# Optimization experiments

Measured on AMD Instinct MI355X. Metric: run time of the kernel, lower is better.

Reference implementation:

```python
import jax, jax.numpy as jnp
import numpy as np

B, C_IN, C_OUT, H, W, K, NK = 16, 256, 256, 64, 64, 3, 2
EPS = 1e-8


def setup_inputs() -> dict:
    key = jax.random.key(0)
    k1, k2, k3, k4 = jax.random.split(key, 4)
    x = jax.random.normal(k1, (B, C_IN, H, W), dtype=jnp.float32)
    mod = jax.random.normal(k2, (B, C_IN), dtype=jnp.float32)
    kernel_mod = jax.random.normal(k3, (B, NK), dtype=jnp.float32)
    # kernel bank: [num_conv_kernels, dim_out, dim_in, k, k] (kaiming-ish scale)
    weights = jax.random.normal(k4, (NK, C_OUT, C_IN, K, K), dtype=jnp.float32) / np.sqrt(C_IN * K * K)
    gamma = jnp.ones((C_OUT,), dtype=jnp.float32)
    return {"x": x, "mod": mod, "kernel_mod": kernel_mod, "weights": weights, "gamma": gamma}


def _block(x, mod, kernel_mod, weights, gamma):
    # adaptive kernel selection: softmax-mix the kernel bank per sample
    attn = jax.nn.softmax(kernel_mod, axis=-1)                       # [b, n]
    w = jnp.einsum('bn,noikl->boikl', attn, weights)                 # [b, o, i, k, k]
    # style modulation over input channels
    w = w * (mod[:, None, :, None, None] + 1.0)
    # demodulation
    denom = jnp.clip(jnp.sum(w * w, axis=(2, 3, 4), keepdims=True), EPS)
    w = w * jax.lax.rsqrt(denom)
    # per-sample conv (groups=b trick in torch) -> vmap over batch
    def conv_one(fmap, wb):
        return jax.lax.conv_general_dilated(
            fmap[None], wb, window_strides=(1, 1), padding='SAME',
            dimension_numbers=('NCHW', 'OIHW', 'NCHW'))[0]
    y = jax.vmap(conv_one)(x, w)                                     # [b, o, h, w]
    # RMSNorm over channel dim: F.normalize(x, dim=1) * gamma * sqrt(dim)
    norm = jnp.sqrt(jnp.sum(y * y, axis=1, keepdims=True))
    y = y / jnp.maximum(norm, 1e-12)
    y = y * gamma[None, :, None, None] * (gamma.shape[0] ** 0.5)
    # SiLU
    return y * jax.nn.sigmoid(y)


def reference(x, mod, kernel_mod, weights, gamma):
    return _block(x, mod, kernel_mod, weights, gamma)
```

## Files before the change

### kernel.cpp

```cpp
#include <hip/hip_runtime.h>
#include <math.h>


typedef __attribute__((ext_vector_type(8))) short short8;
typedef __attribute__((ext_vector_type(16))) float f32x16;

#define GLL16(src, dst)                                                       \
  __builtin_amdgcn_global_load_lds(                                           \
      (const __attribute__((address_space(1))) unsigned int*)(src),           \
      (__attribute__((address_space(3))) unsigned int*)(dst), 16, 0, 0)

static __device__ __forceinline__ unsigned short f2bf(float v) {
  union { float f; unsigned u; } u;
  u.f = v;
  unsigned r = u.u + 0x7FFF + ((u.u >> 16) & 1);
  return (unsigned short)(r >> 16);
}

__global__ __launch_bounds__(256) void wprep(
    const float* __restrict__ mod, const float* __restrict__ kmod,
    const float* __restrict__ weights, unsigned short* __restrict__ wq) {
  int blk = blockIdx.x;
  int b = blk >> 5, oq = blk & 31;
  int t = threadIdx.x;
  int o_l = t >> 5, its = t & 31;
  int o = oq * 8 + o_l;

  float k0 = kmod[b * 2 + 0], k1 = kmod[b * 2 + 1];
  float mx = fmaxf(k0, k1);
  float e0 = expf(k0 - mx), e1 = expf(k1 - mx);
  float ai = 1.0f / (e0 + e1);
  float a0 = e0 * ai, a1 = e1 * ai;

  float wv[9][8];
  float s = 0.0f;
  const float* w0 = &weights[((size_t)o * 256 + its * 8) * 9];
  const float* w1 = w0 + 589824;
#pragma unroll
  for (int e = 0; e < 8; ++e) {
    float f = mod[b * 256 + its * 8 + e] + 1.0f;
#pragma unroll
    for (int j = 0; j < 9; ++j) {
      float v = (a0 * w0[e * 9 + j] + a1 * w1[e * 9 + j]) * f;
      wv[j][e] = v;
      s = fmaf(v, v, s);
    }
  }

  __shared__ float red[8][32];
  __shared__ float scl[8];
  red[o_l][its] = s;
  __syncthreads();
  if (t < 8) {
    float tot = 0.0f;
#pragma unroll
    for (int k = 0; k < 32; ++k) tot += red[t][k];
    scl[t] = rsqrtf(fmaxf(tot, 1e-8f));
  }
  __syncthreads();
  float sc = scl[o_l];

  int c = its >> 1, io = its & 1;
  int oh = o >> 7, mf = (o >> 5) & 3;
  int lane2 = (o & 31) + io * 32;
  size_t cbase = ((size_t)(b * 16 + c)) * 36864 + oh * 2048 + mf * 512 + lane2 * 8;
#pragma unroll
  for (int j = 0; j < 9; ++j) {
    short8 pk;
#pragma unroll
    for (int e = 0; e < 8; ++e) pk[e] = (short)f2bf(wv[j][e] * sc);
    *(short8*)(wq + cbase + j * 4096) = pk;
  }
}

__global__ __launch_bounds__(256) void xprep(
    const float* __restrict__ x, unsigned short* __restrict__ xq) {
  int blk = blockIdx.x;
  int rowp = blk % 66;
  int bc = blk / 66;
  int b = bc >> 4, c = bc & 15;
  int t = threadIdx.x;
  size_t obase = (size_t)blk * 1056;

  if (rowp == 0 || rowp == 65) {
    for (int idx = t; idx < 1056; idx += 256) xq[obase + idx] = 0;
    return;
  }
  __shared__ __align__(16) unsigned short xs2[1056];
  int row = rowp - 1;
  for (int idx = t; idx < 1056; idx += 256) xs2[idx] = 0;
  __syncthreads();
#pragma unroll
  for (int k = 0; k < 4; ++k) {
    int idx = t + k * 256;
    int il = idx >> 6, col = idx & 63;
    float v = x[(((size_t)b * 256 + c * 16 + il) * 64 + row) * 64 + col];
    xs2[(col + 1) * 16 + il] = f2bf(v);
  }
  __syncthreads();
  if (t < 132) *(short8*)(xq + obase + (size_t)t * 8) = *(const short8*)&xs2[t * 8];
}

__global__ __launch_bounds__(256, 2) void conv_fused(
    const unsigned short* __restrict__ xq, const unsigned short* __restrict__ wq,
    const float* __restrict__ gamma, float* __restrict__ out) {
  __shared__ __align__(16) unsigned short xsm[2][6144];
  __shared__ float redl[512];
  __shared__ float invs[128];
  __shared__ float gsm[256];

  int bid = blockIdx.x;
  int xcd = bid & 7;
  int kk = bid >> 3;
  int b = xcd * 2 + (kk >> 5);
  int rt = kk & 31;
  int r0 = rt * 2;

  int t = threadIdx.x;
  int w = t >> 6, lane = t & 63;
  int oh = w & 1, ps = w >> 1;
  int l31 = lane & 31, l5 = lane >> 5;

  gsm[t] = gamma[t];

  int boffs[9];
#pragma unroll
  for (int T = 0; T < 9; ++T) {
    int kh = T / 3, kw = T % 3;
    boffs[T] = (ps + kh) * 2112 + (l31 + kw) * 32 + l5 * 16;
  }

  f32x16 acc[4][2];
#pragma unroll
  for (int mf = 0; mf < 4; ++mf)
#pragma unroll
    for (int h = 0; h < 2; ++h)
#pragma unroll
      for (int q = 0; q < 16; ++q) acc[mf][h][q] = 0.f;

#define GLLX(cn, nb)                                                           \
  _Pragma("unroll") for (int r = 0; r < 3; ++r) {                              \
    GLL16(xq + ((size_t)((b * 16 + (cn)) * 66 + r0)) * 1056 + (r * 256 + t) * 8, \
          &xsm[nb][(r * 256 + t) * 8]);                                        \
  }

#define AGLB(SA, CC, TT)                                                       \
  {                                                                            \
    const unsigned short* ap_ = wq + (size_t)(b * 16 + (CC)) * 36864 +         \
                                (TT) * 4096 + oh * 2048 + lane * 8;            \
    _Pragma("unroll") for (int mf = 0; mf < 4; ++mf)                           \
        SA[mf] = *(const short8*)(ap_ + mf * 512);                             \
  }

#define BDSRD(SB, T, XB)                                                       \
  {                                                                            \
    _Pragma("unroll") for (int h = 0; h < 2; ++h)                              \
        SB[h] = *(const short8*)((XB) + boffs[T] + h * 1024);                  \
  }

#define MFMA8(SA, SB)                                                          \
  {                                                                            \
    __builtin_amdgcn_s_setprio(1);                                             \
    _Pragma("unroll") for (int h = 0; h < 2; ++h)                              \
        _Pragma("unroll") for (int mf = 0; mf < 4; ++mf)                       \
            acc[mf][h] = __builtin_amdgcn_mfma_f32_32x32x16_bf16(              \
                SA[mf], SB[h], acc[mf][h], 0, 0, 0);                           \
    __builtin_amdgcn_s_setprio(0);                                             \
  }

#define SBAR __builtin_amdgcn_sched_barrier(0)
#define LGKM0 asm volatile("s_waitcnt lgkmcnt(0)" ::: "memory")
#define VMC(n) asm volatile("s_waitcnt vmcnt(" #n ")" ::: "memory")
#define BAR __builtin_amdgcn_s_barrier()

  short8 S0[4], S1[4], S2[4], PB[2], QB[2];

  const char* xs0 = (const char*)xsm[0];
  const char* xs1 = (const char*)xsm[1];

  GLLX(0, 0);
  AGLB(S0, 0, 0);
  AGLB(S1, 0, 1);
  AGLB(S2, 0, 2);
  VMC(12);
  BAR;
  SBAR;

  for (int c = 0; c < 16; ++c) {
    const char* XB = (c & 1) ? xs1 : xs0;
    int NB = (c & 1) ^ 1;
    int CN = c < 15 ? c + 1 : 15;
    GLLX(CN, NB);
    BDSRD(PB, 0, XB); SBAR;
    BDSRD(QB, 1, XB); SBAR; MFMA8(S0, PB); AGLB(S0, c, 3); SBAR;
    BDSRD(PB, 2, XB); SBAR; MFMA8(S1, QB); AGLB(S1, c, 4); SBAR;
    BDSRD(QB, 3, XB); SBAR; MFMA8(S2, PB); AGLB(S2, c, 5); SBAR;
    BDSRD(PB, 4, XB); SBAR; MFMA8(S0, QB); AGLB(S0, c, 6); SBAR;
    BDSRD(QB, 5, XB); SBAR; MFMA8(S1, PB); AGLB(S1, c, 7); SBAR;
    BDSRD(PB, 6, XB); SBAR; MFMA8(S2, QB); AGLB(S2, c, 8); SBAR;
    BDSRD(QB, 7, XB); SBAR; MFMA8(S0, PB); AGLB(S0, CN, 0); SBAR;
    BDSRD(PB, 8, XB); SBAR; MFMA8(S1, QB); AGLB(S1, CN, 1); SBAR;
    MFMA8(S2, PB); AGLB(S2, CN, 2); SBAR;
    LGKM0;
    VMC(12);
    BAR;
    SBAR;
  }

#pragma unroll
  for (int h = 0; h < 2; ++h) {
    float pssum = 0.f;
#pragma unroll
    for (int mf = 0; mf < 4; ++mf)
#pragma unroll
      for (int q = 0; q < 16; ++q) {
        float v = acc[mf][h][q];
        pssum = fmaf(v, v, pssum);
      }
    int px = ps * 64 + h * 32 + l31;
    redl[(oh * 2 + l5) * 128 + px] = pssum;
  }
  __syncthreads();
  if (t < 128) {
    float ssum = redl[t] + redl[128 + t] + redl[256 + t] + redl[384 + t];
    invs[t] = 16.0f / fmaxf(sqrtf(ssum), 1e-12f);
  }
  __syncthreads();
  float iv2[2];
#pragma unroll
  for (int h = 0; h < 2; ++h) iv2[h] = invs[ps * 64 + h * 32 + l31];

#pragma unroll
  for (int mf = 0; mf < 4; ++mf)
#pragma unroll
    for (int q = 0; q < 16; ++q) {
      int o = oh * 128 + mf * 32 + (q & 3) + 8 * (q >> 2) + 4 * l5;
      float g = gsm[o];
      size_t ob = ((size_t)b * 256 + o) * 64 + (r0 + ps);
#pragma unroll
      for (int h = 0; h < 2; ++h) {
        float v = acc[mf][h][q] * iv2[h] * g;
        float sg = 1.0f / (1.0f + expf(-v));
        out[ob * 64 + h * 32 + l31] = v * sg;
      }
    }
#undef GLLX
#undef AGLB
#undef BDSRD
#undef MFMA8
#undef SBAR
#undef LGKM0
#undef VMC
#undef BAR
}

extern "C" void kernel_launch(void* const* d_in, const int* in_sizes, int n_in,
                              void* d_out, int out_size, void* d_ws, size_t ws_size,
                              hipStream_t stream) {
  const float* x = (const float*)d_in[0];
  const float* mod = (const float*)d_in[1];
  const float* kmod = (const float*)d_in[2];
  const float* weights = (const float*)d_in[3];
  const float* gamma = (const float*)d_in[4];
  float* out = (float*)d_out;

  unsigned short* xq = (unsigned short*)d_ws;
  unsigned short* wq = (unsigned short*)((char*)d_ws + 35684352);

  wprep<<<512, 256, 0, stream>>>(mod, kmod, weights, wq);
  xprep<<<16 * 16 * 66, 256, 0, stream>>>(x, xq);
  conv_fused<<<512, 256, 0, stream>>>(xq, wq, gamma, out);
}
```

Baseline: 122.5 us.

## Stage four input-channel chunks per LDS buffer and barrier once per group

The conv loop now double-buffers groups of four 16-channel input chunks in LDS instead of single chunks. This cuts workgroup barriers and vmcnt waits from one per chunk to one per group of four. Each chunk load is also trimmed to the 4 padded rows actually read, where the old code copied extra data. In exchange, LDS use per block roughly triples. That could pressure the two-blocks-per-CU occupancy target and makes the vmcnt accounting more delicate.

```diff
diff --git a/kernel.cpp b/kernel.cpp
--- a/kernel.cpp
+++ b/kernel.cpp
@@ -104,7 +104,7 @@
 __global__ __launch_bounds__(256, 2) void conv_fused(
     const unsigned short* __restrict__ xq, const unsigned short* __restrict__ wq,
     const float* __restrict__ gamma, float* __restrict__ out) {
-  __shared__ __align__(16) unsigned short xsm[2][6144];
+  __shared__ __align__(16) unsigned short xsm[2][16896];
   __shared__ float redl[512];
   __shared__ float invs[128];
   __shared__ float gsm[256];
@@ -138,10 +138,14 @@
 #pragma unroll
       for (int q = 0; q < 16; ++q) acc[mf][h][q] = 0.f;
 
-#define GLLX(cn, nb)                                                           \
-  _Pragma("unroll") for (int r = 0; r < 3; ++r) {                              \
-    GLL16(xq + ((size_t)((b * 16 + (cn)) * 66 + r0)) * 1056 + (r * 256 + t) * 8, \
-          &xsm[nb][(r * 256 + t) * 8]);                                        \
+#define GLLXC(cn, nb, ch)                                                      \
+  {                                                                            \
+    const unsigned short* sp_ =                                                \
+        xq + ((size_t)((b * 16 + (cn)) * 66 + r0)) * 1056;                     \
+    unsigned short* dp_ = &xsm[nb][(ch) * 4224];                               \
+    GLL16(sp_ + t * 8, dp_ + t * 8);                                           \
+    GLL16(sp_ + (256 + t) * 8, dp_ + (256 + t) * 8);                           \
+    if (t < 16) GLL16(sp_ + (512 + t) * 8, dp_ + (512 + t) * 8);               \
   }
 
 #define AGLB(SA, CC, TT)                                                       \
@@ -175,10 +179,7 @@
 
   short8 S0[4], S1[4], S2[4], PB[2], QB[2];
 
-  const char* xs0 = (const char*)xsm[0];
-  const char* xs1 = (const char*)xsm[1];
-
-  GLLX(0, 0);
+  GLLXC(0, 0, 0); GLLXC(1, 0, 1); GLLXC(2, 0, 2); GLLXC(3, 0, 3);
   AGLB(S0, 0, 0);
   AGLB(S1, 0, 1);
   AGLB(S2, 0, 2);
@@ -186,25 +187,31 @@
   BAR;
   SBAR;
 
-  for (int c = 0; c < 16; ++c) {
-    const char* XB = (c & 1) ? xs1 : xs0;
-    int NB = (c & 1) ^ 1;
-    int CN = c < 15 ? c + 1 : 15;
-    GLLX(CN, NB);
-    BDSRD(PB, 0, XB); SBAR;
-    BDSRD(QB, 1, XB); SBAR; MFMA8(S0, PB); AGLB(S0, c, 3); SBAR;
-    BDSRD(PB, 2, XB); SBAR; MFMA8(S1, QB); AGLB(S1, c, 4); SBAR;
-    BDSRD(QB, 3, XB); SBAR; MFMA8(S2, PB); AGLB(S2, c, 5); SBAR;
-    BDSRD(PB, 4, XB); SBAR; MFMA8(S0, QB); AGLB(S0, c, 6); SBAR;
-    BDSRD(QB, 5, XB); SBAR; MFMA8(S1, PB); AGLB(S1, c, 7); SBAR;
-    BDSRD(PB, 6, XB); SBAR; MFMA8(S2, QB); AGLB(S2, c, 8); SBAR;
-    BDSRD(QB, 7, XB); SBAR; MFMA8(S0, PB); AGLB(S0, CN, 0); SBAR;
-    BDSRD(PB, 8, XB); SBAR; MFMA8(S1, QB); AGLB(S1, CN, 1); SBAR;
-    MFMA8(S2, PB); AGLB(S2, CN, 2); SBAR;
-    LGKM0;
-    VMC(12);
-    BAR;
-    SBAR;
+  for (int s2 = 0; s2 < 4; ++s2) {
+    const char* XBb = (const char*)xsm[s2 & 1];
+    int nb = (s2 & 1) ^ 1;
+    for (int i = 0; i < 4; ++i) {
+      int c = s2 * 4 + i;
+      int CN = c < 15 ? c + 1 : 15;
+      if (s2 < 3) GLLXC(c + 4, nb, i);
+      const char* XB = XBb + i * 8448;
+      BDSRD(PB, 0, XB); SBAR;
+      BDSRD(QB, 1, XB); SBAR; MFMA8(S0, PB); AGLB(S0, c, 3); SBAR;
+      BDSRD(PB, 2, XB); SBAR; MFMA8(S1, QB); AGLB(S1, c, 4); SBAR;
+      BDSRD(QB, 3, XB); SBAR; MFMA8(S2, PB); AGLB(S2, c, 5); SBAR;
+      BDSRD(PB, 4, XB); SBAR; MFMA8(S0, QB); AGLB(S0, c, 6); SBAR;
+      BDSRD(QB, 5, XB); SBAR; MFMA8(S1, PB); AGLB(S1, c, 7); SBAR;
+      BDSRD(PB, 6, XB); SBAR; MFMA8(S2, QB); AGLB(S2, c, 8); SBAR;
+      BDSRD(QB, 7, XB); SBAR; MFMA8(S0, PB); AGLB(S0, CN, 0); SBAR;
+      BDSRD(PB, 8, XB); SBAR; MFMA8(S1, QB); AGLB(S1, CN, 1); SBAR;
+      MFMA8(S2, PB); AGLB(S2, CN, 2); SBAR;
+    }
+    if (s2 < 3) {
+      LGKM0;
+      VMC(36);
+      BAR;
+      SBAR;
+    }
   }
 
 #pragma unroll
@@ -244,7 +251,7 @@
         out[ob * 64 + h * 32 + l31] = v * sg;
       }
     }
-#undef GLLX
+#undef GLLXC
 #undef AGLB
 #undef BDSRD
 #undef MFMA8
```

Result: slower. 125.2 us (+2.2%).
